# Performance work log

Measured on AMD Instinct MI355X. Metric: run time of the kernel, lower is better.

Reference implementation:

```python
import jax, jax.numpy as jnp
import numpy as np
from jax import lax

D_MODEL, D_STATE, D_CONV, EXPAND, HEADDIM = 1024, 128, 4, 2, 64
D_INNER = EXPAND * D_MODEL            # 2048
NHEADS = D_INNER // HEADDIM           # 32
CONV_DIM = D_INNER + 2 * D_STATE      # 2304 (ngroups=1)
D_IN_PROJ = 2 * D_INNER + 2 * D_STATE + NHEADS  # 4384


def setup_inputs() -> dict:
    key = jax.random.key(0)
    ks = jax.random.split(key, 9)
    b, l = 2, 2048
    x = jax.random.normal(ks[0], (b, l, D_MODEL), jnp.float32)
    in_proj_w = jax.random.normal(ks[1], (D_IN_PROJ, D_MODEL), jnp.float32) * 0.02
    conv_w = jax.random.normal(ks[2], (CONV_DIM, D_CONV), jnp.float32) * 0.2
    conv_b = jax.random.normal(ks[3], (CONV_DIM,), jnp.float32) * 0.02
    dt_bias = jnp.log(jnp.expm1(jax.random.uniform(ks[4], (NHEADS,), jnp.float32, 0.001, 0.1)))
    A_log = jnp.log(jax.random.uniform(ks[5], (NHEADS,), jnp.float32, 1.0, 16.0))
    D = jax.random.normal(ks[6], (NHEADS,), jnp.float32)
    norm_w = jnp.ones((D_INNER,), jnp.float32)
    out_proj_w = jax.random.normal(ks[7], (D_MODEL, D_INNER), jnp.float32) * 0.02
    return {"x": x, "in_proj_w": in_proj_w, "conv_w": conv_w, "conv_b": conv_b,
            "dt_bias": dt_bias, "A_log": A_log, "D": D, "norm_w": norm_w,
            "out_proj_w": out_proj_w}


def _mamba2(x, in_proj_w, conv_w, conv_b, dt_bias, A_log, D, norm_w, out_proj_w):
    b, l, _ = x.shape
    zxbcdt = x @ in_proj_w.T  # (b,l,D_IN_PROJ)
    z = zxbcdt[..., :D_INNER]
    xBC = zxbcdt[..., D_INNER:D_INNER + CONV_DIM]
    dt = zxbcdt[..., D_INNER + CONV_DIM:]  # (b,l,h)
    # causal depthwise conv1d + SiLU
    xBC_pad = jnp.pad(xBC, ((0, 0), (D_CONV - 1, 0), (0, 0)))
    windows = jnp.stack([xBC_pad[:, k:k + l, :] for k in range(D_CONV)], axis=-1)  # (b,l,c,K)
    xBC = jax.nn.silu(jnp.einsum('blck,ck->blc', windows, conv_w) + conv_b)
    xs = xBC[..., :D_INNER]
    B = xBC[..., D_INNER:D_INNER + D_STATE]   # (b,l,n)
    C = xBC[..., D_INNER + D_STATE:]          # (b,l,n)
    xh = xs.reshape(b, l, NHEADS, HEADDIM)
    dt = jax.nn.softplus(dt + dt_bias)        # (b,l,h)
    A = -jnp.exp(A_log)                       # (h,)
    dA = jnp.exp(dt * A)                      # (b,l,h)
    xdt = xh * dt[..., None]                  # (b,l,h,p)

    def step(S, inp):
        dA_t, xdt_t, B_t, C_t = inp  # (b,h),(b,h,p),(b,n),(b,n)
        S = dA_t[:, :, None, None] * S + xdt_t[..., None] * B_t[:, None, None, :]
        y_t = jnp.einsum('bhpn,bn->bhp', S, C_t)
        return S, y_t

    S0 = jnp.zeros((b, NHEADS, HEADDIM, D_STATE), x.dtype)
    _, y = lax.scan(step, S0,
                    (dA.transpose(1, 0, 2), xdt.transpose(1, 0, 2, 3),
                     B.transpose(1, 0, 2), C.transpose(1, 0, 2)))
    y = y.transpose(1, 0, 2, 3) + D[None, None, :, None] * xh  # (b,l,h,p)
    y = y.reshape(b, l, D_INNER)
    # gated RMSNorm: norm(y * silu(z)) * weight
    y = y * jax.nn.silu(z)
    y = y * lax.rsqrt(jnp.mean(y * y, axis=-1, keepdims=True) + 1e-5) * norm_w
    return y @ out_proj_w.T


def reference(x, in_proj_w, conv_w, conv_b, dt_bias, A_log, D, norm_w, out_proj_w):
    return x + _mamba2(x, in_proj_w, conv_w, conv_b, dt_bias, A_log, D, norm_w, out_proj_w)
```

## Files before the change

### kernel.cpp

```cpp
#include <hip/hip_runtime.h>
#include <hip/hip_bf16.h>
#include <cstdint>

typedef __hip_bfloat16 bf16;
typedef __attribute__((ext_vector_type(8))) short short8;
typedef __attribute__((ext_vector_type(4))) float f32x4;
typedef unsigned int u32;

#define BB 2
#define LL 2048
#define DM 1024
#define DI 2048
#define DS 128
#define NH 32
#define HD 64
#define CONVD 2304
#define DPROJ 4384
#define DPAD 4480
#define NBL (BB*LL)
#define NCHK 16
#define CLEN 128

__device__ __forceinline__ float bf2f(bf16 v) { return __bfloat162float(v); }
__device__ __forceinline__ bf16 f2bf(float f) { return __float2bfloat16(f); }
__device__ __forceinline__ unsigned short f2bfu(float f) {
  bf16 t = __float2bfloat16(f); return *(unsigned short*)&t;
}
__device__ __forceinline__ float bfu2f(unsigned short u) {
  u32 b = ((u32)u) << 16; return *(float*)&b;
}

__device__ __forceinline__ void gload16(const void* g, void* l) {
  __builtin_amdgcn_global_load_lds(
      (const __attribute__((address_space(1))) u32*)g,
      (__attribute__((address_space(3))) u32*)l, 16, 0, 0);
}

__global__ __launch_bounds__(256)
void k_cast3(const float* __restrict__ s0, bf16* __restrict__ d0, int n0,
             const float* __restrict__ s1, bf16* __restrict__ d1, int n1,
             const float* __restrict__ s2, bf16* __restrict__ d2, int n2)
{
  int i = blockIdx.x * blockDim.x + threadIdx.x;
  const int stride = gridDim.x * blockDim.x;
  const int total = n0 + n1 + n2;
  for (; i < total; i += stride) {
    const float* s; bf16* d; int j = i;
    if (j < n0)            { s = s0; d = d0; }
    else if (j < n0 + n1)  { s = s1; d = d1; j -= n0; }
    else                   { s = s2; d = d2; j -= n0 + n1; }
    const float4 v = ((const float4*)s)[j];
    u32 w0 = (u32)f2bfu(v.x) | ((u32)f2bfu(v.y) << 16);
    u32 w1 = (u32)f2bfu(v.z) | ((u32)f2bfu(v.w) << 16);
    *(uint2*)(d + (size_t)j*4) = make_uint2(w0, w1);
  }
}

template<int TM, int MODE>
__global__ __launch_bounds__(512)
void k_gemm_nt(const bf16* __restrict__ A, const bf16* __restrict__ W,
               int K, int Nw, int ldo,
               float* __restrict__ outf, const bf16* __restrict__ residb,
               bf16* __restrict__ outb, float* __restrict__ dtraw)
{
  __shared__ __align__(16) unsigned short S[(TM + 128) * 64];
  unsigned short* As = S;
  unsigned short* Ws = S + TM*64;
  const int tid = threadIdx.x;
  const int w = tid >> 6, lane = tid & 63;
  const int m0 = blockIdx.x * TM, n0 = blockIdx.y * 128;
  const int wr = w >> 2, wc = w & 3;
  constexpr int MI = TM / 32;
  f32x4 acc[MI][2] = {};
  const int r0 = lane & 15;
  const int kq = (lane >> 4) * 8;

  for (int k0 = 0; k0 < K; k0 += 64) {
    #pragma unroll
    for (int it = 0; it < TM/64; ++it) {
      const int seg = it*8 + w;
      const int idx = seg*512 + lane*8;
      const int row = idx >> 6, col = idx & 63;
      gload16(A + (size_t)(m0 + row)*K + (k0 + col), (char*)As + seg*1024);
    }
    #pragma unroll
    for (int it = 0; it < 2; ++it) {
      const int seg = it*8 + w;
      const int idx = seg*512 + lane*8;
      const int row = idx >> 6, col = idx & 63;
      int rw = n0 + row; rw = (rw < Nw) ? rw : (Nw - 1);
      gload16(W + (size_t)rw*K + (k0 + col), (char*)Ws + seg*1024);
    }
    __syncthreads();
    #pragma unroll
    for (int kk = 0; kk < 64; kk += 32) {
      short8 af[MI], bw[2];
      #pragma unroll
      for (int mi = 0; mi < MI; ++mi)
        af[mi] = *(const short8*)(As + (wr*(TM/2) + mi*16 + r0)*64 + kk + kq);
      #pragma unroll
      for (int ni = 0; ni < 2; ++ni)
        bw[ni] = *(const short8*)(Ws + (wc*32 + ni*16 + r0)*64 + kk + kq);
      #pragma unroll
      for (int mi = 0; mi < MI; ++mi)
        #pragma unroll
        for (int ni = 0; ni < 2; ++ni)
          acc[mi][ni] = __builtin_amdgcn_mfma_f32_16x16x32_bf16(af[mi], bw[ni], acc[mi][ni], 0, 0, 0);
    }
    __syncthreads();
  }
  const int rr = (lane >> 4) * 4;
  if (MODE == 0) {
    #pragma unroll
    for (int mi = 0; mi < MI; ++mi) {
      #pragma unroll
      for (int ni = 0; ni < 2; ++ni) {
        const int col = n0 + wc*32 + ni*16 + r0;
        #pragma unroll
        for (int r = 0; r < 4; ++r) {
          const int row = m0 + wr*(TM/2) + mi*16 + rr + r;
          outf[(size_t)row*ldo + col] =
              acc[mi][ni][r] + bf2f(residb[(size_t)row*ldo + col]);
        }
      }
    }
  } else {
    if (n0 == 4352 && wc == 0) {
      #pragma unroll
      for (int ni = 0; ni < 2; ++ni)
        #pragma unroll
        for (int mi = 0; mi < MI; ++mi)
          #pragma unroll
          for (int r = 0; r < 4; ++r) {
            const int row = m0 + wr*(TM/2) + mi*16 + rr + r;
            dtraw[(size_t)row*NH + ni*16 + r0] = acc[mi][ni][r];
          }
    }
    #pragma unroll
    for (int mi = 0; mi < MI; ++mi) {
      #pragma unroll
      for (int ni = 0; ni < 2; ++ni) {
        const int colt = wc*32 + ni*16 + r0;
        #pragma unroll
        for (int r = 0; r < 4; ++r) {
          const int rowt = wr*(TM/2) + mi*16 + rr + r;
          const int g = (colt >> 3) ^ (rowt & 7);
          S[rowt*128 + g*8 + (colt & 7)] = f2bfu(acc[mi][ni][r]);
        }
      }
    }
    __syncthreads();
    const int row = tid >> 2, j4 = tid & 3;
    unsigned short* orow = (unsigned short*)outb + (size_t)(m0 + row)*ldo + n0 + j4*32;
    #pragma unroll
    for (int jj = 0; jj < 4; ++jj) {
      const int g = (j4*4 + jj) ^ (row & 7);
      *(short8*)(orow + jj*8) = *(const short8*)&S[row*128 + g*8];
    }
  }
}

__global__ __launch_bounds__(256)
void k_conv(const bf16* __restrict__ zxb, const float* __restrict__ dtraw,
            const float* __restrict__ convw, const float* __restrict__ convb,
            const float* __restrict__ dtb, const float* __restrict__ alog,
            bf16* __restrict__ xs, float* __restrict__ dt,
            float* __restrict__ ldA, bf16* __restrict__ Bc, bf16* __restrict__ Cc)
{
  const int bl = blockIdx.x;
  const int l = bl & (LL - 1);
  const int tid = threadIdx.x;
  if (tid < NH) {
    float raw = dtraw[(size_t)bl*NH + tid] + dtb[tid];
    float sp = (raw > 20.f) ? raw : log1pf(__expf(raw));
    float Ah = -__expf(alog[tid]);
    dt[(size_t)bl*NH + tid] = sp;
    ldA[(size_t)bl*NH + tid] = sp * Ah;
  }
  for (int g = tid; g < CONVD/8; g += 256) {
    const int c0 = g*8;
    float acc[8];
    float4 wv[8];
    #pragma unroll
    for (int e = 0; e < 8; ++e) wv[e] = ((const float4*)convw)[c0 + e];
    {
      const float4 b0 = *(const float4*)(convb + c0);
      const float4 b1 = *(const float4*)(convb + c0 + 4);
      acc[0]=b0.x; acc[1]=b0.y; acc[2]=b0.z; acc[3]=b0.w;
      acc[4]=b1.x; acc[5]=b1.y; acc[6]=b1.z; acc[7]=b1.w;
    }
    #pragma unroll
    for (int k = 0; k < 4; ++k) {
      if (l - 3 + k >= 0) {
        short8 v = *(const short8*)((const unsigned short*)zxb + (size_t)(bl - 3 + k)*DPAD + DI + c0);
        #pragma unroll
        for (int e = 0; e < 8; ++e) {
          const float wk = (k == 0) ? wv[e].x : (k == 1) ? wv[e].y : (k == 2) ? wv[e].z : wv[e].w;
          acc[e] = fmaf(bfu2f((unsigned short)v[e]), wk, acc[e]);
        }
      }
    }
    short8 ov;
    #pragma unroll
    for (int e = 0; e < 8; ++e) {
      const float s = acc[e] / (1.f + __expf(-acc[e]));
      ov[e] = (short)f2bfu(s);
    }
    if (c0 < DI)            *(short8*)((unsigned short*)xs + (size_t)bl*DI + c0) = ov;
    else if (c0 < DI + DS)  *(short8*)((unsigned short*)Bc + (size_t)bl*DS + (c0 - DI)) = ov;
    else                    *(short8*)((unsigned short*)Cc + (size_t)bl*DS + (c0 - DI - DS)) = ov;
  }
}

__global__ __launch_bounds__(256)
void k_bt(const bf16* __restrict__ Bc, bf16* __restrict__ BT)
{
  const int bidx2 = blockIdx.x;
  const int b = bidx2 >> 4, c = bidx2 & 15;
  const int bl0 = b*LL + c*CLEN;
  __shared__ unsigned short LT[128*132];
  const int tid = threadIdx.x;
  {
    const int ts = tid >> 3, seg = tid & 7;
    #pragma unroll
    for (int r = 0; r < 4; ++r) {
      const int t = r*32 + ts;
      const unsigned short* src = (const unsigned short*)(Bc + (size_t)(bl0 + t)*DS);
      short8 v0 = *(const short8*)(src + seg*16);
      short8 v1 = *(const short8*)(src + seg*16 + 8);
      u32 w0 = (u32)(unsigned short)v0[0] | ((u32)(unsigned short)v0[1] << 16);
      u32 w1 = (u32)(unsigned short)v0[2] | ((u32)(unsigned short)v0[3] << 16);
      u32 w2 = (u32)(unsigned short)v0[4] | ((u32)(unsigned short)v0[5] << 16);
      u32 w3 = (u32)(unsigned short)v0[6] | ((u32)(unsigned short)v0[7] << 16);
      u32 w4 = (u32)(unsigned short)v1[0] | ((u32)(unsigned short)v1[1] << 16);
      u32 w5 = (u32)(unsigned short)v1[2] | ((u32)(unsigned short)v1[3] << 16);
      u32 w6 = (u32)(unsigned short)v1[4] | ((u32)(unsigned short)v1[5] << 16);
      u32 w7 = (u32)(unsigned short)v1[6] | ((u32)(unsigned short)v1[7] << 16);
      uint2* d = (uint2*)&LT[t*132 + seg*16];
      d[0] = make_uint2(w0, w1); d[1] = make_uint2(w2, w3);
      d[2] = make_uint2(w4, w5); d[3] = make_uint2(w6, w7);
    }
  }
  __syncthreads();
  {
    const int n = tid >> 1, th = tid & 1;
    unsigned short* dst = (unsigned short*)(BT + (size_t)bidx2*16384 + n*128 + th*64);
    #pragma unroll
    for (int j = 0; j < 8; ++j) {
      short8 o;
      #pragma unroll
      for (int e = 0; e < 8; ++e)
        o[e] = (short)LT[(th*64 + j*8 + e)*132 + n];
      *(short8*)(dst + j*8) = o;
    }
  }
}

__global__ __launch_bounds__(512)
void k_xt_state(const bf16* __restrict__ xs, const float* __restrict__ dt,
                const bf16* __restrict__ BT, const float* __restrict__ ldA,
                bf16* __restrict__ xT, unsigned short* __restrict__ Sloc,
                float* __restrict__ clog)
{
  const int bidx = blockIdx.x;
  const int c = bidx & 15, h = (bidx >> 4) & 31, b = bidx >> 9;
  const int bl0 = b*LL + c*CLEN;
  const int bidx2 = b*NCHK + c;
  __shared__ unsigned short LT[128*68];
  __shared__ __align__(16) unsigned short BTs[128*136];
  __shared__ __align__(16) unsigned short XWs[64*136];
  __shared__ float w1[128];
  const int tid = threadIdx.x;
  {
    const int ts = tid >> 3, seg = tid & 7;
    #pragma unroll
    for (int r = 0; r < 2; ++r) {
      const int t = r*64 + ts;
      const float dtv = dt[(size_t)(bl0 + t)*NH + h];
      short8 v = *(const short8*)((const unsigned short*)(xs + (size_t)(bl0 + t)*DI + h*HD) + seg*8);
      unsigned short o[8];
      #pragma unroll
      for (int e = 0; e < 8; ++e)
        o[e] = f2bfu(bfu2f((unsigned short)v[e]) * dtv);
      uint2* d = (uint2*)&LT[t*68 + seg*8];
      d[0] = make_uint2((u32)o[0] | ((u32)o[1] << 16), (u32)o[2] | ((u32)o[3] << 16));
      d[1] = make_uint2((u32)o[4] | ((u32)o[5] << 16), (u32)o[6] | ((u32)o[7] << 16));
    }
  }
  {
    const int n = tid >> 2, sg = tid & 3;
    const unsigned short* src = (const unsigned short*)(BT + (size_t)bidx2*16384 + n*128 + sg*32);
    #pragma unroll
    for (int j = 0; j < 4; ++j)
      *(short8*)&BTs[n*136 + sg*32 + j*8] = *(const short8*)(src + j*8);
  }
  if (tid < 64) {
    const int ln = tid;
    const float a0 = ldA[(size_t)(bl0 + 2*ln)*NH + h];
    const float a1 = ldA[(size_t)(bl0 + 2*ln + 1)*NH + h];
    float s = a0 + a1;
    #pragma unroll
    for (int off = 1; off < 64; off <<= 1) {
      const float v = __shfl_up(s, off);
      if (ln >= off) s += v;
    }
    const float Ltot = __shfl(s, 63);
    w1[2*ln + 1] = __expf(Ltot - s);
    w1[2*ln]     = __expf(Ltot - (s - a1));
    if (ln == 63) clog[bidx] = Ltot;
  }
  __syncthreads();
  {
    const int p = tid >> 3, tg = tid & 7;
    unsigned short* xdst = (unsigned short*)xT + (size_t)bidx*8192 + p*128 + tg*16;
    #pragma unroll
    for (int half = 0; half < 2; ++half) {
      short8 oXT, oXW;
      #pragma unroll
      for (int e = 0; e < 8; ++e) {
        const int t = tg*16 + half*8 + e;
        const unsigned short u = LT[t*68 + p];
        oXT[e] = (short)u;
        oXW[e] = (short)f2bfu(bfu2f(u) * w1[t]);
      }
      *(short8*)(xdst + half*8) = oXT;
      *(short8*)&XWs[p*136 + tg*16 + half*8] = oXW;
    }
  }
  __syncthreads();
  const int w = tid >> 6, lane = tid & 63;
  const int r0 = lane & 15, kq = (lane >> 4) * 8;
  f32x4 acc[4] = {};
  #pragma unroll
  for (int kk = 0; kk < 4; ++kk) {
    short8 bfrag = *(const short8*)&BTs[(w*16 + r0)*136 + kk*32 + kq];
    #pragma unroll
    for (int mi = 0; mi < 4; ++mi) {
      short8 a = *(const short8*)&XWs[(mi*16 + r0)*136 + kk*32 + kq];
      acc[mi] = __builtin_amdgcn_mfma_f32_16x16x32_bf16(a, bfrag, acc[mi], 0, 0, 0);
    }
  }
  const int rr = (lane >> 4) * 4;
  unsigned short* So = Sloc + (size_t)bidx*8192;
  #pragma unroll
  for (int mi = 0; mi < 4; ++mi)
    #pragma unroll
    for (int r = 0; r < 4; ++r)
      So[(mi*16 + rr + r)*128 + w*16 + r0] = f2bfu(acc[mi][r]);
}

__global__ __launch_bounds__(256)
void k_chunk_combine(unsigned short* __restrict__ Sloc, const float* __restrict__ clog)
{
  const int bh = blockIdx.x >> 3;
  const int e0 = ((blockIdx.x & 7) * 256 + threadIdx.x) * 4;
  float t0 = 0.f, t1 = 0.f, t2 = 0.f, t3 = 0.f;
  for (int c = 0; c < NCHK; ++c) {
    unsigned short* Sp = Sloc + ((size_t)(bh*NCHK + c))*8192 + e0;
    const uint2 raw = *(const uint2*)Sp;
    const float l0 = bfu2f((unsigned short)(raw.x & 0xffff));
    const float l1 = bfu2f((unsigned short)(raw.x >> 16));
    const float l2 = bfu2f((unsigned short)(raw.y & 0xffff));
    const float l3 = bfu2f((unsigned short)(raw.y >> 16));
    uint2 o;
    o.x = (u32)f2bfu(t0) | ((u32)f2bfu(t1) << 16);
    o.y = (u32)f2bfu(t2) | ((u32)f2bfu(t3) << 16);
    *(uint2*)Sp = o;
    const float P = __expf(clog[bh*NCHK + c]);
    t0 = P*t0 + l0; t1 = P*t1 + l1; t2 = P*t2 + l2; t3 = P*t3 + l3;
  }
}

__global__ __launch_bounds__(512)
void k_scan(const bf16* __restrict__ xT, const bf16* __restrict__ Bc,
            const bf16* __restrict__ Cc, const unsigned short* __restrict__ Sinit,
            const float* __restrict__ ldA, const bf16* __restrict__ xs,
            const float* __restrict__ Dv, unsigned short* __restrict__ y)
{
  const int bidx = blockIdx.x;
  const int c = bidx & 15, h = (bidx >> 4) & 31, b = bidx >> 9;
  const int bl0 = b*LL + c*CLEN;
  __shared__ __align__(16) unsigned short Cs[128*136];
  __shared__ __align__(16) unsigned short Bs[128*136];
  __shared__ __align__(16) unsigned short XDs[64*136];
  __shared__ __align__(16) unsigned short SIs[64*136];
  __shared__ float la[128];
  const int tid = threadIdx.x;
  {
    const int t = tid >> 2, sg = tid & 3;
    const unsigned short* sc = (const unsigned short*)(Cc + (size_t)(bl0 + t)*DS) + sg*32;
    const unsigned short* sb = (const unsigned short*)(Bc + (size_t)(bl0 + t)*DS) + sg*32;
    #pragma unroll
    for (int j = 0; j < 4; ++j) {
      *(short8*)&Cs[t*136 + sg*32 + j*8] = *(const short8*)(sc + j*8);
      *(short8*)&Bs[t*136 + sg*32 + j*8] = *(const short8*)(sb + j*8);
    }
  }
  {
    const int p = tid >> 3, seg = tid & 7;
    const unsigned short* sx = (const unsigned short*)(xT + (size_t)bidx*8192 + p*128) + seg*16;
    *(short8*)&XDs[p*136 + seg*16]     = *(const short8*)sx;
    *(short8*)&XDs[p*136 + seg*16 + 8] = *(const short8*)(sx + 8);
    const unsigned short* sp = Sinit + (size_t)bidx*8192 + p*128 + seg*16;
    *(short8*)&SIs[p*136 + seg*16]     = *(const short8*)sp;
    *(short8*)&SIs[p*136 + seg*16 + 8] = *(const short8*)(sp + 8);
  }
  if (tid < 64) {
    const int ln = tid;
    const float a0 = ldA[(size_t)(bl0 + 2*ln)*NH + h];
    const float a1 = ldA[(size_t)(bl0 + 2*ln + 1)*NH + h];
    float s = a0 + a1;
    #pragma unroll
    for (int off = 1; off < 64; off <<= 1) {
      const float v = __shfl_up(s, off);
      if (ln >= off) s += v;
    }
    la[2*ln + 1] = s;
    la[2*ln]     = s - a1;
  }
  __syncthreads();

  const int w = tid >> 6, lane = tid & 63;
  const int r0 = lane & 15, kq = (lane >> 4) * 8;
  const int trow = w*16 + (lane >> 4) * 4;

  f32x4 aG[8] = {};
  f32x4 aU[4] = {};
  #pragma unroll
  for (int kk = 0; kk < 4; ++kk) {
    short8 a = *(const short8*)&Cs[(w*16 + r0)*136 + kk*32 + kq];
    #pragma unroll
    for (int sf = 0; sf < 8; ++sf) {
      short8 bb = *(const short8*)&Bs[(sf*16 + r0)*136 + kk*32 + kq];
      aG[sf] = __builtin_amdgcn_mfma_f32_16x16x32_bf16(a, bb, aG[sf], 0, 0, 0);
    }
    #pragma unroll
    for (int pf = 0; pf < 4; ++pf) {
      short8 bs = *(const short8*)&SIs[(pf*16 + r0)*136 + kk*32 + kq];
      aU[pf] = __builtin_amdgcn_mfma_f32_16x16x32_bf16(a, bs, aU[pf], 0, 0, 0);
    }
  }
  __syncthreads();
  float lat[4];
  #pragma unroll
  for (int r = 0; r < 4; ++r) lat[r] = la[trow + r];
  #pragma unroll
  for (int sf = 0; sf < 8; ++sf) {
    const int s = sf*16 + r0;
    const float las = la[s];
    #pragma unroll
    for (int r = 0; r < 4; ++r) {
      const int t = trow + r;
      const float m = (s <= t) ? aG[sf][r] * __expf(lat[r] - las) : 0.f;
      Bs[t*136 + s] = f2bfu(m);
    }
  }
  __syncthreads();
  f32x4 aY[4] = {};
  #pragma unroll
  for (int kk = 0; kk < 4; ++kk) {
    short8 a = *(const short8*)&Bs[(w*16 + r0)*136 + kk*32 + kq];
    #pragma unroll
    for (int pf = 0; pf < 4; ++pf) {
      short8 bx = *(const short8*)&XDs[(pf*16 + r0)*136 + kk*32 + kq];
      aY[pf] = __builtin_amdgcn_mfma_f32_16x16x32_bf16(a, bx, aY[pf], 0, 0, 0);
    }
  }
  const float Dh = Dv[h];
  float el[4];
  #pragma unroll
  for (int r = 0; r < 4; ++r) el[r] = __expf(lat[r]);
  #pragma unroll
  for (int pf = 0; pf < 4; ++pf) {
    #pragma unroll
    for (int r = 0; r < 4; ++r) {
      const int t = trow + r, p = pf*16 + r0;
      const size_t gi = (size_t)(bl0 + t)*DI + h*HD + p;
      const float yv = aY[pf][r] + el[r]*aU[pf][r] + Dh*bfu2f(((const unsigned short*)xs)[gi]);
      y[gi] = f2bfu(yv);
    }
  }
}

__global__ __launch_bounds__(256)
void k_gate_norm(const unsigned short* __restrict__ y, const bf16* __restrict__ zxb,
                 const float* __restrict__ nw, bf16* __restrict__ yn)
{
  const size_t bl = blockIdx.x;
  const int tid = threadIdx.x;
  const int c0 = tid * 8;
  short8 yv8 = *(const short8*)(y + bl*DI + c0);
  short8 zv = *(const short8*)((const unsigned short*)zxb + bl*DPAD + c0);
  float v[8];
  float acc = 0.f;
  #pragma unroll
  for (int e = 0; e < 8; ++e) {
    const float zf = bfu2f((unsigned short)zv[e]);
    v[e] = bfu2f((unsigned short)yv8[e]) * (zf / (1.f + __expf(-zf)));
    acc += v[e]*v[e];
  }
  #pragma unroll
  for (int off = 32; off > 0; off >>= 1) acc += __shfl_down(acc, off);
  __shared__ float red[4];
  if ((tid & 63) == 0) red[tid >> 6] = acc;
  __syncthreads();
  const float total = red[0] + red[1] + red[2] + red[3];
  const float r = rsqrtf(total * (1.f/DI) + 1e-5f);
  const float4 w0 = *(const float4*)(nw + c0);
  const float4 w1 = *(const float4*)(nw + c0 + 4);
  const float wv[8] = {w0.x, w0.y, w0.z, w0.w, w1.x, w1.y, w1.z, w1.w};
  short8 ov;
  #pragma unroll
  for (int e = 0; e < 8; ++e) ov[e] = (short)f2bfu(v[e] * r * wv[e]);
  *(short8*)((unsigned short*)yn + bl*DI + c0) = ov;
}

extern "C" void kernel_launch(void* const* d_in, const int* in_sizes, int n_in,
                              void* d_out, int out_size, void* d_ws, size_t ws_size,
                              hipStream_t stream)
{
  const float* x     = (const float*)d_in[0];
  const float* inw   = (const float*)d_in[1];
  const float* convw = (const float*)d_in[2];
  const float* convb = (const float*)d_in[3];
  const float* dtb   = (const float*)d_in[4];
  const float* alog  = (const float*)d_in[5];
  const float* Dv    = (const float*)d_in[6];
  const float* nw    = (const float*)d_in[7];
  const float* outw  = (const float*)d_in[8];
  float* out = (float*)d_out;
  char* ws = (char*)d_ws;

  constexpr size_t OFF_ZX   = 0;
  constexpr size_t OFF_DTRAW= OFF_ZX   + (size_t)NBL*DPAD*2;
  constexpr size_t OFF_XS   = OFF_DTRAW+ (size_t)NBL*NH*4;
  constexpr size_t OFF_DT   = OFF_XS   + (size_t)NBL*DI*2;
  constexpr size_t OFF_LDA  = OFF_DT   + (size_t)NBL*NH*4;
  constexpr size_t OFF_B    = OFF_LDA  + (size_t)NBL*NH*4;
  constexpr size_t OFF_C    = OFF_B    + (size_t)NBL*DS*2;
  constexpr size_t OFF_XT   = OFF_C    + (size_t)NBL*DS*2;
  constexpr size_t OFF_BT   = OFF_XT   + (size_t)1024*8192*2;
  constexpr size_t OFF_SLOC = OFF_BT   + (size_t)32*16384*2;
  constexpr size_t OFF_CLOG = OFF_SLOC + (size_t)1024*8192*2;
  constexpr size_t OFF_Y    = OFF_CLOG + 4096;
  constexpr size_t OFF_YN   = OFF_Y    + (size_t)NBL*DI*2;
  constexpr size_t OFF_XB   = OFF_YN   + (size_t)NBL*DI*2;
  constexpr size_t OFF_INWB = OFF_XB   + (size_t)NBL*DM*2;
  constexpr size_t OFF_OUTWB= OFF_INWB + (size_t)DPROJ*DM*2;

  bf16*  zxb  = (bf16*) (ws + OFF_ZX);
  float* dtraw= (float*)(ws + OFF_DTRAW);
  bf16*  xs   = (bf16*) (ws + OFF_XS);
  float* dt   = (float*)(ws + OFF_DT);
  float* ldA  = (float*)(ws + OFF_LDA);
  bf16*  Bcp  = (bf16*) (ws + OFF_B);
  bf16*  Ccp  = (bf16*) (ws + OFF_C);
  bf16*  xT   = (bf16*) (ws + OFF_XT);
  bf16*  BT   = (bf16*) (ws + OFF_BT);
  unsigned short* Sloc = (unsigned short*)(ws + OFF_SLOC);
  float* clog = (float*)(ws + OFF_CLOG);
  unsigned short* yb = (unsigned short*)(ws + OFF_Y);
  bf16*  yn   = (bf16*) (ws + OFF_YN);
  bf16*  xb   = (bf16*) (ws + OFF_XB);
  bf16*  inwb = (bf16*) (ws + OFF_INWB);
  bf16*  outwb= (bf16*) (ws + OFF_OUTWB);

  k_cast3<<<2048, 256, 0, stream>>>(x, xb, NBL*DM/4,
                                    inw, inwb, DPROJ*DM/4,
                                    outw, outwb, DM*DI/4);
  k_gemm_nt<128,1><<<dim3(32, 35), 512, 0, stream>>>(xb, inwb, DM, DPROJ, DPAD, nullptr, nullptr, zxb, dtraw);
  k_conv<<<NBL, 256, 0, stream>>>(zxb, dtraw, convw, convb, dtb, alog, xs, dt, ldA, Bcp, Ccp);
  k_bt<<<BB*NCHK, 256, 0, stream>>>(Bcp, BT);
  k_xt_state<<<BB*NH*NCHK, 512, 0, stream>>>(xs, dt, BT, ldA, xT, Sloc, clog);
  k_chunk_combine<<<64*8, 256, 0, stream>>>(Sloc, clog);
  k_scan<<<BB*NH*NCHK, 512, 0, stream>>>(xT, Bcp, Ccp, Sloc, ldA, xs, Dv, yb);
  k_gate_norm<<<NBL, 256, 0, stream>>>(yb, zxb, nw, yn);
  k_gemm_nt<64,0><<<dim3(64, 8), 512, 0, stream>>>(yn, outwb, DI, DM, DM, out, xb, nullptr, nullptr);
}
```

Measured before the change: 240.6 us.

## Double-buffer GEMM LDS tiles and XOR-swizzle shared layout

Measured after the change: 204.7 us. 14.9% less time.

```diff
diff --git a/kernel.cpp b/kernel.cpp
--- a/kernel.cpp
+++ b/kernel.cpp
@@ -63,9 +63,8 @@
                float* __restrict__ outf, const bf16* __restrict__ residb,
                bf16* __restrict__ outb, float* __restrict__ dtraw)
 {
-  __shared__ __align__(16) unsigned short S[(TM + 128) * 64];
-  unsigned short* As = S;
-  unsigned short* Ws = S + TM*64;
+  constexpr int BUFE = (TM + 128) * 64;
+  __shared__ __align__(16) unsigned short S[2*BUFE];
   const int tid = threadIdx.x;
   const int w = tid >> 6, lane = tid & 63;
   const int m0 = blockIdx.x * TM, n0 = blockIdx.y * 128;
@@ -74,33 +73,62 @@
   f32x4 acc[MI][2] = {};
   const int r0 = lane & 15;
   const int kq = (lane >> 4) * 8;
-
-  for (int k0 = 0; k0 < K; k0 += 64) {
+  const int srow = lane >> 3;
+  const int scol = ((lane & 7) ^ (lane >> 3)) << 3;
+  const int swz  = (r0 & 7) << 3;
+  const int NT = K >> 6;
+
+  {
+    unsigned short* dst = S;
     #pragma unroll
     for (int it = 0; it < TM/64; ++it) {
       const int seg = it*8 + w;
-      const int idx = seg*512 + lane*8;
-      const int row = idx >> 6, col = idx & 63;
-      gload16(A + (size_t)(m0 + row)*K + (k0 + col), (char*)As + seg*1024);
-    }
+      const int row = seg*8 + srow;
+      gload16(A + (size_t)(m0 + row)*K + scol, (char*)dst + seg*1024);
+    }
+    unsigned short* dstW = dst + TM*64;
     #pragma unroll
     for (int it = 0; it < 2; ++it) {
       const int seg = it*8 + w;
-      const int idx = seg*512 + lane*8;
-      const int row = idx >> 6, col = idx & 63;
+      const int row = seg*8 + srow;
       int rw = n0 + row; rw = (rw < Nw) ? rw : (Nw - 1);
-      gload16(W + (size_t)rw*K + (k0 + col), (char*)Ws + seg*1024);
-    }
-    __syncthreads();
+      gload16(W + (size_t)rw*K + scol, (char*)dstW + seg*1024);
+    }
+  }
+  __syncthreads();
+
+  for (int t = 0; t < NT; ++t) {
+    const int cur = t & 1;
+    if (t + 1 < NT) {
+      const int k0 = (t + 1) << 6;
+      unsigned short* dst = S + (cur ^ 1) * BUFE;
+      #pragma unroll
+      for (int it = 0; it < TM/64; ++it) {
+        const int seg = it*8 + w;
+        const int row = seg*8 + srow;
+        gload16(A + (size_t)(m0 + row)*K + (k0 + scol), (char*)dst + seg*1024);
+      }
+      unsigned short* dstW = dst + TM*64;
+      #pragma unroll
+      for (int it = 0; it < 2; ++it) {
+        const int seg = it*8 + w;
+        const int row = seg*8 + srow;
+        int rw = n0 + row; rw = (rw < Nw) ? rw : (Nw - 1);
+        gload16(W + (size_t)rw*K + (k0 + scol), (char*)dstW + seg*1024);
+      }
+    }
+    const unsigned short* As = S + cur*BUFE;
+    const unsigned short* Ws = As + TM*64;
     #pragma unroll
     for (int kk = 0; kk < 64; kk += 32) {
+      const int ce = (kk + kq) ^ swz;
       short8 af[MI], bw[2];
       #pragma unroll
       for (int mi = 0; mi < MI; ++mi)
-        af[mi] = *(const short8*)(As + (wr*(TM/2) + mi*16 + r0)*64 + kk + kq);
+        af[mi] = *(const short8*)(As + (wr*(TM/2) + mi*16 + r0)*64 + ce);
       #pragma unroll
       for (int ni = 0; ni < 2; ++ni)
-        bw[ni] = *(const short8*)(Ws + (wc*32 + ni*16 + r0)*64 + kk + kq);
+        bw[ni] = *(const short8*)(Ws + (wc*32 + ni*16 + r0)*64 + ce);
       #pragma unroll
       for (int mi = 0; mi < MI; ++mi)
         #pragma unroll
@@ -109,6 +137,7 @@
     }
     __syncthreads();
   }
+
   const int rr = (lane >> 4) * 4;
   if (MODE == 0) {
     #pragma unroll
```

## Double-buffer GEMM LDS tiles with XOR swizzle; load B/C fragments directly to registers

Applied to the files above, without the earlier changes.

After: 194.5 us. 19.1% less time.

```diff
diff --git a/kernel.cpp b/kernel.cpp
--- a/kernel.cpp
+++ b/kernel.cpp
@@ -36,6 +36,19 @@
       (__attribute__((address_space(3))) u32*)l, 16, 0, 0);
 }
 
+template<int N> __device__ __forceinline__ void waitvm() {
+  __builtin_amdgcn_sched_barrier(0);
+  if constexpr (N == 0) asm volatile("s_waitcnt vmcnt(0)" ::: "memory");
+  else if constexpr (N == 3) asm volatile("s_waitcnt vmcnt(3)" ::: "memory");
+  else if constexpr (N == 4) asm volatile("s_waitcnt vmcnt(4)" ::: "memory");
+  __builtin_amdgcn_sched_barrier(0);
+}
+__device__ __forceinline__ void rawbar() {
+  __builtin_amdgcn_sched_barrier(0);
+  __builtin_amdgcn_s_barrier();
+  __builtin_amdgcn_sched_barrier(0);
+}
+
 __global__ __launch_bounds__(256)
 void k_cast3(const float* __restrict__ s0, bf16* __restrict__ d0, int n0,
              const float* __restrict__ s1, bf16* __restrict__ d1, int n1,
@@ -63,9 +76,9 @@
                float* __restrict__ outf, const bf16* __restrict__ residb,
                bf16* __restrict__ outb, float* __restrict__ dtraw)
 {
-  __shared__ __align__(16) unsigned short S[(TM + 128) * 64];
-  unsigned short* As = S;
-  unsigned short* Ws = S + TM*64;
+  constexpr int BUFE = (TM + 128) * 64;
+  constexpr int LPT  = TM/64 + 2;
+  __shared__ __align__(16) unsigned short S[2*BUFE];
   const int tid = threadIdx.x;
   const int w = tid >> 6, lane = tid & 63;
   const int m0 = blockIdx.x * TM, n0 = blockIdx.y * 128;
@@ -74,41 +87,67 @@
   f32x4 acc[MI][2] = {};
   const int r0 = lane & 15;
   const int kq = (lane >> 4) * 8;
-
-  for (int k0 = 0; k0 < K; k0 += 64) {
-    #pragma unroll
-    for (int it = 0; it < TM/64; ++it) {
-      const int seg = it*8 + w;
-      const int idx = seg*512 + lane*8;
-      const int row = idx >> 6, col = idx & 63;
-      gload16(A + (size_t)(m0 + row)*K + (k0 + col), (char*)As + seg*1024);
-    }
-    #pragma unroll
-    for (int it = 0; it < 2; ++it) {
-      const int seg = it*8 + w;
-      const int idx = seg*512 + lane*8;
-      const int row = idx >> 6, col = idx & 63;
-      int rw = n0 + row; rw = (rw < Nw) ? rw : (Nw - 1);
-      gload16(W + (size_t)rw*K + (k0 + col), (char*)Ws + seg*1024);
-    }
-    __syncthreads();
+  const int srow = lane >> 3;
+  const int scol = ((lane & 7) ^ (lane >> 3)) << 3;
+  const int swz  = (r0 & 7) << 3;
+  const int NT = K >> 6;
+
+#define STAGE(T, BUF) {                                                          \
+    const int k0s = (T) << 6;                                                    \
+    unsigned short* dst = S + (BUF) * BUFE;                                      \
+    _Pragma("unroll")                                                            \
+    for (int it = 0; it < TM/64; ++it) {                                         \
+      const int seg = it*8 + w;                                                  \
+      const int row = seg*8 + srow;                                              \
+      gload16(A + (size_t)(m0 + row)*K + (k0s + scol), (char*)dst + seg*1024);   \
+    }                                                                            \
+    unsigned short* dstW = dst + TM*64;                                          \
+    _Pragma("unroll")                                                            \
+    for (int it = 0; it < 2; ++it) {                                             \
+      const int seg = it*8 + w;                                                  \
+      const int row = seg*8 + srow;                                              \
+      int rw = n0 + row; rw = (rw < Nw) ? rw : (Nw - 1);                         \
+      gload16(W + (size_t)rw*K + (k0s + scol), (char*)dstW + seg*1024);          \
+    }                                                                            \
+  }
+
+  STAGE(0, 0);
+  STAGE(1, 1);
+  waitvm<LPT>();
+  rawbar();
+
+  for (int t = 0; t < NT; ++t) {
+    const int cur = t & 1;
+    const unsigned short* As = S + cur*BUFE;
+    const unsigned short* Ws = As + TM*64;
     #pragma unroll
     for (int kk = 0; kk < 64; kk += 32) {
+      const int ce = (kk + kq) ^ swz;
       short8 af[MI], bw[2];
       #pragma unroll
       for (int mi = 0; mi < MI; ++mi)
-        af[mi] = *(const short8*)(As + (wr*(TM/2) + mi*16 + r0)*64 + kk + kq);
+        af[mi] = *(const short8*)(As + (wr*(TM/2) + mi*16 + r0)*64 + ce);
       #pragma unroll
       for (int ni = 0; ni < 2; ++ni)
-        bw[ni] = *(const short8*)(Ws + (wc*32 + ni*16 + r0)*64 + kk + kq);
+        bw[ni] = *(const short8*)(Ws + (wc*32 + ni*16 + r0)*64 + ce);
       #pragma unroll
       for (int mi = 0; mi < MI; ++mi)
         #pragma unroll
         for (int ni = 0; ni < 2; ++ni)
           acc[mi][ni] = __builtin_amdgcn_mfma_f32_16x16x32_bf16(af[mi], bw[ni], acc[mi][ni], 0, 0, 0);
     }
-    __syncthreads();
-  }
+    rawbar();
+    if (t + 2 < NT) {
+      STAGE(t + 2, cur);
+      waitvm<LPT>();
+      rawbar();
+    } else if (t + 1 < NT) {
+      waitvm<0>();
+      rawbar();
+    }
+  }
+#undef STAGE
+
   const int rr = (lane >> 4) * 4;
   if (MODE == 0) {
     #pragma unroll
@@ -267,10 +306,16 @@
   const int bl0 = b*LL + c*CLEN;
   const int bidx2 = b*NCHK + c;
   __shared__ unsigned short LT[128*68];
-  __shared__ __align__(16) unsigned short BTs[128*136];
   __shared__ __align__(16) unsigned short XWs[64*136];
   __shared__ float w1[128];
   const int tid = threadIdx.x;
+  const int w = tid >> 6, lane = tid & 63;
+  const int r0 = lane & 15, kq = (lane >> 4) * 8;
+  short8 bfr[4];
+  #pragma unroll
+  for (int kk = 0; kk < 4; ++kk)
+    bfr[kk] = *(const short8*)((const unsigned short*)BT + (size_t)bidx2*16384
+                               + (size_t)(w*16 + r0)*128 + kk*32 + kq);
   {
     const int ts = tid >> 3, seg = tid & 7;
     #pragma unroll
@@ -286,13 +331,6 @@
       d[0] = make_uint2((u32)o[0] | ((u32)o[1] << 16), (u32)o[2] | ((u32)o[3] << 16));
       d[1] = make_uint2((u32)o[4] | ((u32)o[5] << 16), (u32)o[6] | ((u32)o[7] << 16));
     }
-  }
-  {
-    const int n = tid >> 2, sg = tid & 3;
-    const unsigned short* src = (const unsigned short*)(BT + (size_t)bidx2*16384 + n*128 + sg*32);
-    #pragma unroll
-    for (int j = 0; j < 4; ++j)
-      *(short8*)&BTs[n*136 + sg*32 + j*8] = *(const short8*)(src + j*8);
   }
   if (tid < 64) {
     const int ln = tid;
@@ -328,16 +366,13 @@
     }
   }
   __syncthreads();
-  const int w = tid >> 6, lane = tid & 63;
-  const int r0 = lane & 15, kq = (lane >> 4) * 8;
   f32x4 acc[4] = {};
   #pragma unroll
   for (int kk = 0; kk < 4; ++kk) {
-    short8 bfrag = *(const short8*)&BTs[(w*16 + r0)*136 + kk*32 + kq];
     #pragma unroll
     for (int mi = 0; mi < 4; ++mi) {
       short8 a = *(const short8*)&XWs[(mi*16 + r0)*136 + kk*32 + kq];
-      acc[mi] = __builtin_amdgcn_mfma_f32_16x16x32_bf16(a, bfrag, acc[mi], 0, 0, 0);
+      acc[mi] = __builtin_amdgcn_mfma_f32_16x16x32_bf16(a, bfr[kk], acc[mi], 0, 0, 0);
     }
   }
   const int rr = (lane >> 4) * 4;
@@ -380,21 +415,24 @@
   const int bidx = blockIdx.x;
   const int c = bidx & 15, h = (bidx >> 4) & 31, b = bidx >> 9;
   const int bl0 = b*LL + c*CLEN;
-  __shared__ __align__(16) unsigned short Cs[128*136];
   __shared__ __align__(16) unsigned short Bs[128*136];
   __shared__ __align__(16) unsigned short XDs[64*136];
   __shared__ __align__(16) unsigned short SIs[64*136];
   __shared__ float la[128];
   const int tid = threadIdx.x;
+  const int w = tid >> 6, lane = tid & 63;
+  const int r0 = lane & 15, kq = (lane >> 4) * 8;
+  short8 cfr[4];
+  #pragma unroll
+  for (int kk = 0; kk < 4; ++kk)
+    cfr[kk] = *(const short8*)((const unsigned short*)Cc
+                               + (size_t)(bl0 + w*16 + r0)*DS + kk*32 + kq);
   {
     const int t = tid >> 2, sg = tid & 3;
-    const unsigned short* sc = (const unsigned short*)(Cc + (size_t)(bl0 + t)*DS) + sg*32;
     const unsigned short* sb = (const unsigned short*)(Bc + (size_t)(bl0 + t)*DS) + sg*32;
     #pragma unroll
-    for (int j = 0; j < 4; ++j) {
-      *(short8*)&Cs[t*136 + sg*32 + j*8] = *(const short8*)(sc + j*8);
+    for (int j = 0; j < 4; ++j)
       *(short8*)&Bs[t*136 + sg*32 + j*8] = *(const short8*)(sb + j*8);
-    }
   }
   {
     const int p = tid >> 3, seg = tid & 7;
@@ -420,24 +458,21 @@
   }
   __syncthreads();
 
-  const int w = tid >> 6, lane = tid & 63;
-  const int r0 = lane & 15, kq = (lane >> 4) * 8;
   const int trow = w*16 + (lane >> 4) * 4;
 
   f32x4 aG[8] = {};
   f32x4 aU[4] = {};
   #pragma unroll
   for (int kk = 0; kk < 4; ++kk) {
-    short8 a = *(const short8*)&Cs[(w*16 + r0)*136 + kk*32 + kq];
     #pragma unroll
     for (int sf = 0; sf < 8; ++sf) {
       short8 bb = *(const short8*)&Bs[(sf*16 + r0)*136 + kk*32 + kq];
-      aG[sf] = __builtin_amdgcn_mfma_f32_16x16x32_bf16(a, bb, aG[sf], 0, 0, 0);
+      aG[sf] = __builtin_amdgcn_mfma_f32_16x16x32_bf16(cfr[kk], bb, aG[sf], 0, 0, 0);
     }
     #pragma unroll
     for (int pf = 0; pf < 4; ++pf) {
       short8 bs = *(const short8*)&SIs[(pf*16 + r0)*136 + kk*32 + kq];
-      aU[pf] = __builtin_amdgcn_mfma_f32_16x16x32_bf16(a, bs, aU[pf], 0, 0, 0);
+      aU[pf] = __builtin_amdgcn_mfma_f32_16x16x32_bf16(cfr[kk], bs, aU[pf], 0, 0, 0);
     }
   }
   __syncthreads();
```
